# Kernel optimization log

Hardware: AMD Instinct MI355X
Metric: run time of the kernel (lower is better)

Reference implementation:

```python
import jax, jax.numpy as jnp
import numpy as np

EPS = 1e-8
BLOCK = 10  # proposals per frame; block-diagonal zeroing granularity


def _l2norm(x):
    # torch.norm(x, dim=-1, keepdim=True) + 1e-8
    return x / (jnp.linalg.norm(x, axis=-1, keepdims=True) + EPS)


def _block_mask(N):
    # For row j: zero cols [ (j//10)*10 , (j//10)*10 + 9 ) (i.e. 9 cols), then restore the diagonal.
    rows = jnp.arange(N)[:, None]
    cols = jnp.arange(N)[None, :]
    bstart = (rows // BLOCK) * BLOCK
    zeroed = (cols >= bstart) & (cols < bstart + (BLOCK - 1))
    keep = (~zeroed) | (rows == cols)
    return keep.astype(jnp.float32)  # [N, N]


def setup_inputs() -> dict:
    key = jax.random.key(0)
    k1, k2, k3, k4 = jax.random.split(key, 4)
    B, N, C = 1, 2000, 256
    x_cls = jax.random.normal(k1, (B, N, C), dtype=jnp.float32)
    x_reg = jax.random.normal(k2, (B, N, C), dtype=jnp.float32)
    s = 1.0 / np.sqrt(C)
    W_qkv_cls = jax.random.uniform(k3, (C, 3 * C), dtype=jnp.float32, minval=-s, maxval=s)
    W_qkv_reg = jax.random.uniform(k4, (C, 3 * C), dtype=jnp.float32, minval=-s, maxval=s)
    return {"x_cls": x_cls, "x_reg": x_reg, "W_qkv_cls": W_qkv_cls, "W_qkv_reg": W_qkv_reg}


def reference(x_cls, x_reg, W_qkv_cls, W_qkv_reg):
    num_heads = 8
    scale = 25.0
    sim_thresh = 0.75
    B, N, C = x_cls.shape
    hd = C // num_heads

    def qkv(x, W):
        # [B,N,3C] -> (3,B,H,N,hd)
        t = (x @ W).reshape(B, N, 3, num_heads, hd)
        return jnp.transpose(t, (2, 0, 3, 1, 4))

    q_cls, k_cls, v_cls = qkv(x_cls, W_qkv_cls)
    q_reg, k_reg, _v_reg = qkv(x_reg, W_qkv_reg)

    q_cls = _l2norm(q_cls)
    k_cls = _l2norm(k_cls)
    q_reg = _l2norm(q_reg)
    k_reg = _l2norm(k_reg)
    v_cls_normed = _l2norm(v_cls)

    # cosine-similarity of values (used for sim mask)
    attn_cls_raw = jnp.einsum('bhnd,bhmd->bhnm', v_cls_normed, v_cls_normed)

    attn_cls = jax.nn.softmax(jnp.einsum('bhnd,bhmd->bhnm', q_cls, k_cls) * scale, axis=-1)
    attn_reg = jax.nn.softmax(jnp.einsum('bhnd,bhmd->bhnm', q_reg, k_reg) * scale, axis=-1)
    attn = (attn_reg + attn_cls) * 0.5

    # block-diagonal zeroing (keeps diagonal), replacing the original CPU/numpy loop
    attn = attn * _block_mask(N)[None, None, :, :]

    x = jnp.einsum('bhnm,bhmd->bhnd', attn, v_cls)
    x = jnp.transpose(x, (0, 2, 1, 3)).reshape(B, N, C)
    x_ori = jnp.transpose(v_cls, (0, 2, 1, 3)).reshape(B, N, C)
    x_out = jnp.concatenate([x, x_ori], axis=-1)  # [B, N, 2C]

    # ave=True branch
    raw_mean = jnp.sum(attn_cls_raw, axis=1)[0] / num_heads          # [N, N]
    sim_mask = (raw_mean > sim_thresh).astype(jnp.float32)
    sim_attn = jnp.sum(attn, axis=1)[0] / num_heads                   # [N, N]
    sim_round2 = jax.nn.softmax(sim_attn, axis=-1)
    sim_round2 = sim_mask * sim_round2 / (jnp.sum(sim_mask * sim_round2, axis=-1, keepdims=True) + EPS)

    return (x_out, sim_round2)
```

## Files before the change

### kernel.cpp

```cpp
#include <hip/hip_runtime.h>
#include <math.h>

#define N_TOK 2000
#define NH 8
#define NHH 2
#define HD 32
#define SCALE 25.0f
#define SIM_TH 0.75f
#define EPSF 1e-8f
#define NT 125
#define QT 16

typedef _Float16 half2_t __attribute__((ext_vector_type(2)));
typedef _Float16 f16x4 __attribute__((ext_vector_type(4)));
typedef _Float16 f16x8 __attribute__((ext_vector_type(8)));
typedef float f32x4 __attribute__((ext_vector_type(4)));

__device__ __forceinline__ half2_t u2h(unsigned u) {
  return __builtin_bit_cast(half2_t, u);
}
__device__ __forceinline__ unsigned h2u(half2_t h) {
  return __builtin_bit_cast(unsigned, h);
}

__device__ __forceinline__ float block_max256(float v, float* red) {
#pragma unroll
  for (int off = 32; off > 0; off >>= 1) v = fmaxf(v, __shfl_xor(v, off, 64));
  __syncthreads();
  if ((threadIdx.x & 63) == 0) red[threadIdx.x >> 6] = v;
  __syncthreads();
  return fmaxf(fmaxf(red[0], red[1]), fmaxf(red[2], red[3]));
}
__device__ __forceinline__ float block_sum256(float v, float* red) {
#pragma unroll
  for (int off = 32; off > 0; off >>= 1) v += __shfl_xor(v, off, 64);
  __syncthreads();
  if ((threadIdx.x & 63) == 0) red[threadIdx.x >> 6] = v;
  __syncthreads();
  return (red[0] + red[1]) + (red[2] + red[3]);
}

__global__ __launch_bounds__(256) void wpackT_kernel(
    const float* __restrict__ W_cls, const float* __restrict__ W_reg,
    _Float16* __restrict__ Wt_cls, _Float16* __restrict__ Wt_reg) {
  const int idx = blockIdx.x * 256 + threadIdx.x;
  const int kc = idx / 768;
  const int n = idx % 768;
  const float* __restrict__ W = blockIdx.y ? W_reg : W_cls;
  _Float16* __restrict__ Wt = blockIdx.y ? Wt_reg : Wt_cls;
  uint4 o;
  o.x = h2u((half2_t){(_Float16)W[(kc * 8 + 0) * 768 + n],
                      (_Float16)W[(kc * 8 + 1) * 768 + n]});
  o.y = h2u((half2_t){(_Float16)W[(kc * 8 + 2) * 768 + n],
                      (_Float16)W[(kc * 8 + 3) * 768 + n]});
  o.z = h2u((half2_t){(_Float16)W[(kc * 8 + 4) * 768 + n],
                      (_Float16)W[(kc * 8 + 5) * 768 + n]});
  o.w = h2u((half2_t){(_Float16)W[(kc * 8 + 6) * 768 + n],
                      (_Float16)W[(kc * 8 + 7) * 768 + n]});
  *(uint4*)(Wt + (size_t)n * 256 + kc * 8) = o;
}

__global__ __launch_bounds__(256) void qkv_mfma_kernel(
    const float* __restrict__ x_cls, const float* __restrict__ x_reg,
    const _Float16* __restrict__ Wt_cls, const _Float16* __restrict__ Wt_reg,
    _Float16* __restrict__ qc2, _Float16* __restrict__ qr2,
    _Float16* __restrict__ kc2, _Float16* __restrict__ kr2,
    _Float16* __restrict__ vn2, float* __restrict__ v_rm,
    _Float16* __restrict__ v_t) {
  __shared__ _Float16 xs[16][264];

  const int tid = threadIdx.x;
  const int c = blockIdx.y;
  const int which = (c >= 3) ? 1 : 0;
  const int sec = which ? (c - 3) : c;
  const int n0 = sec * 256;
  const int i0 = blockIdx.x * 16;
  const float* __restrict__ x = which ? x_reg : x_cls;
  const _Float16* __restrict__ Wt = which ? Wt_reg : Wt_cls;

  {
    const int tok = tid >> 4, c4 = tid & 15;
    const float4* __restrict__ xr =
        (const float4*)(x + (size_t)(i0 + tok) * 256);
#pragma unroll
    for (int r = 0; r < 4; r++) {
      const float4 v = xr[c4 + 16 * r];
      *(unsigned*)&xs[tok][(c4 + 16 * r) * 4] =
          h2u((half2_t){(_Float16)v.x, (_Float16)v.y});
      *(unsigned*)&xs[tok][(c4 + 16 * r) * 4 + 2] =
          h2u((half2_t){(_Float16)v.z, (_Float16)v.w});
    }
  }
  __syncthreads();

  const int w = tid >> 6, l = tid & 63;
  const int q = l & 15, kg = l >> 4;
  const f32x4 zero4 = {0.f, 0.f, 0.f, 0.f};
  f32x4 acc[4] = {zero4, zero4, zero4, zero4};
  const int nb = n0 + w * 64;

#pragma unroll
  for (int ks = 0; ks < 8; ks++) {
    const int k0 = ks * 32;
    const f16x8 bx = *(const f16x8*)&xs[q][k0 + kg * 8];
#pragma unroll
    for (int t2 = 0; t2 < 4; t2++) {
      const f16x8 aw = *(const f16x8*)(
          Wt + (size_t)(nb + t2 * 16 + q) * 256 + k0 + kg * 8);
      acc[t2] =
          __builtin_amdgcn_mfma_f32_16x16x32_f16(aw, bx, acc[t2], 0, 0, 0);
    }
  }

  float ss0 = 0.f, ss1 = 0.f;
#pragma unroll
  for (int i = 0; i < 4; i++) {
    ss0 += acc[0][i] * acc[0][i] + acc[1][i] * acc[1][i];
    ss1 += acc[2][i] * acc[2][i] + acc[3][i] * acc[3][i];
  }
  ss0 += __shfl_xor(ss0, 16, 64);
  ss0 += __shfl_xor(ss0, 32, 64);
  ss1 += __shfl_xor(ss1, 16, 64);
  ss1 += __shfl_xor(ss1, 32, 64);
  const float inv0 = 1.0f / (sqrtf(ss0) + EPSF);
  const float inv1 = 1.0f / (sqrtf(ss1) + EPSF);

  const int tok = i0 + q;
#pragma unroll
  for (int t2 = 0; t2 < 4; t2++) {
    const float inv = (t2 < 2) ? inv0 : inv1;
    const int nrel = w * 64 + t2 * 16 + kg * 4;
    const int h = nrel >> 5, d0 = nrel & 31;
    uint2 un;
    un.x = h2u((half2_t){(_Float16)(acc[t2][0] * inv),
                         (_Float16)(acc[t2][1] * inv)});
    un.y = h2u((half2_t){(_Float16)(acc[t2][2] * inv),
                         (_Float16)(acc[t2][3] * inv)});
    const size_t off = ((size_t)(h * N_TOK) + tok) * 32 + d0;
    if (sec == 0) {
      *(uint2*)((which ? qr2 : qc2) + off) = un;
    } else if (sec == 1) {
      *(uint2*)((which ? kr2 : kc2) + off) = un;
    } else {
      *(uint2*)(vn2 + off) = un;
      const float4 vr = {acc[t2][0], acc[t2][1], acc[t2][2], acc[t2][3]};
      *(float4*)(v_rm + off) = vr;
#pragma unroll
      for (int i = 0; i < 4; i++) {
        v_t[((size_t)(h * 32) + d0 + i) * N_TOK + tok] = (_Float16)acc[t2][i];
      }
    }
  }
}

__global__ __launch_bounds__(256) void attn33_kernel(
    const _Float16* __restrict__ qc2, const _Float16* __restrict__ qr2,
    const _Float16* __restrict__ kc2, const _Float16* __restrict__ kr2,
    const _Float16* __restrict__ vn2, const _Float16* __restrict__ v_t,
    const float* __restrict__ v_rm, float* __restrict__ out_x,
    _Float16* __restrict__ sim_ws, _Float16* __restrict__ raw_ws) {
  __shared__ _Float16 qst[3][NHH][QT][40];
  __shared__ float smem_u[4224];

  float* __restrict__ sums_l = smem_u;
  float* __restrict__ nrm = smem_u + 256;
  float* __restrict__ st = smem_u;
  float* __restrict__ pvr = smem_u;

  const int tid = threadIdx.x;
  const int w = tid >> 6;
  const int l = tid & 63;
  const int qgrp = blockIdx.x >> 2;
  const int hp = blockIdx.x & 3;
  const int hq = hp * NHH;
  const int i0 = qgrp * QT;
  _Float16* __restrict__ simp = sim_ws + (size_t)hp * N_TOK * N_TOK;
  _Float16* __restrict__ rawp = raw_ws + (size_t)hp * N_TOK * N_TOK;

  if (tid < 128) {
    const int hh = tid >> 6, row = (tid >> 2) & 15, dg = tid & 3;
    const size_t src =
        ((size_t)((hq + hh) * N_TOK) + (i0 + row)) * HD + dg * 8;
    *(uint4*)&qst[0][hh][row][dg * 8] = *(const uint4*)(qc2 + src);
    *(uint4*)&qst[1][hh][row][dg * 8] = *(const uint4*)(qr2 + src);
    *(uint4*)&qst[2][hh][row][dg * 8] = *(const uint4*)(vn2 + src);
  }
  __syncthreads();

  const int q = l & 15;
  const int kg = l >> 4;
  const int i_glob = i0 + q;
  const int bs = (i_glob / 10) * 10;

  const f32x4 zero4 = {0.f, 0.f, 0.f, 0.f};

  float sc[NHH], sr[NHH];
#pragma unroll
  for (int hh = 0; hh < NHH; hh++) { sc[hh] = 0.f; sr[hh] = 0.f; }

  for (int t = w; t < NT; t += 4) {
    const int mb = t * 16;
#pragma unroll
    for (int hh = 0; hh < NHH; hh++) {
      const size_t koff =
          ((size_t)((hq + hh) * N_TOK) + mb + q) * HD + kg * 8;
      const f16x8 akc = *(const f16x8*)(kc2 + koff);
      const f16x8 akr = *(const f16x8*)(kr2 + koff);
      const f16x8 bqc = *(const f16x8*)&qst[0][hh][q][kg * 8];
      const f16x8 bqr = *(const f16x8*)&qst[1][hh][q][kg * 8];
      const f32x4 dc =
          __builtin_amdgcn_mfma_f32_16x16x32_f16(akc, bqc, zero4, 0, 0, 0);
      const f32x4 dr =
          __builtin_amdgcn_mfma_f32_16x16x32_f16(akr, bqr, zero4, 0, 0, 0);
#pragma unroll
      for (int i = 0; i < 4; i++) {
        sc[hh] += __expf(dc[i] * SCALE - SCALE);
        sr[hh] += __expf(dr[i] * SCALE - SCALE);
      }
    }
  }
#pragma unroll
  for (int hh = 0; hh < NHH; hh++) {
    sc[hh] += __shfl_xor(sc[hh], 16, 64);
    sc[hh] += __shfl_xor(sc[hh], 32, 64);
    sr[hh] += __shfl_xor(sr[hh], 16, 64);
    sr[hh] += __shfl_xor(sr[hh], 32, 64);
  }
  if (l < 16) {
#pragma unroll
    for (int hh = 0; hh < NHH; hh++) {
      sums_l[((w * 2 + 0) * NHH + hh) * 16 + l] = sc[hh];
      sums_l[((w * 2 + 1) * NHH + hh) * 16 + l] = sr[hh];
    }
  }
  __syncthreads();
  if (tid < 64) {
    const int pl = tid >> 5, hh = (tid >> 4) & 1, qq = tid & 15;
    const float s = sums_l[((0 * 2 + pl) * NHH + hh) * 16 + qq] +
                    sums_l[((1 * 2 + pl) * NHH + hh) * 16 + qq] +
                    sums_l[((2 * 2 + pl) * NHH + hh) * 16 + qq] +
                    sums_l[((3 * 2 + pl) * NHH + hh) * 16 + qq];
    nrm[(pl * NHH + hh) * 16 + qq] = 0.5f / s;
  }
  __syncthreads();
  float ncr[NHH], nrr[NHH];
#pragma unroll
  for (int hh = 0; hh < NHH; hh++) {
    ncr[hh] = nrm[(0 * NHH + hh) * 16 + q];
    nrr[hh] = nrm[(1 * NHH + hh) * 16 + q];
  }
  __syncthreads();

  f32x4 pv[NHH][2];
#pragma unroll
  for (int hh = 0; hh < NHH; hh++) { pv[hh][0] = zero4; pv[hh][1] = zero4; }

  for (int t = w; t < NT; t += 4) {
    const int mb = t * 16;
    f32x4 simt = zero4;
    f32x4 rawt = zero4;
#pragma unroll
    for (int hh = 0; hh < NHH; hh++) {
      const int h = hq + hh;
      const size_t koff = ((size_t)(h * N_TOK) + mb + q) * HD + kg * 8;
      const f16x8 akc = *(const f16x8*)(kc2 + koff);
      const f16x8 akr = *(const f16x8*)(kr2 + koff);
      const f16x8 avn = *(const f16x8*)(vn2 + koff);
      const f16x8 bqc = *(const f16x8*)&qst[0][hh][q][kg * 8];
      const f16x8 bqr = *(const f16x8*)&qst[1][hh][q][kg * 8];
      const f16x8 bqv = *(const f16x8*)&qst[2][hh][q][kg * 8];
      const f32x4 dc =
          __builtin_amdgcn_mfma_f32_16x16x32_f16(akc, bqc, zero4, 0, 0, 0);
      const f32x4 dr =
          __builtin_amdgcn_mfma_f32_16x16x32_f16(akr, bqr, zero4, 0, 0, 0);
      rawt = __builtin_amdgcn_mfma_f32_16x16x32_f16(avn, bqv, rawt, 0, 0, 0);

      f16x4 pa;
#pragma unroll
      for (int i = 0; i < 4; i++) {
        const float ec = __expf(dc[i] * SCALE - SCALE);
        const float er = __expf(dr[i] * SCALE - SCALE);
        float ai = ncr[hh] * ec + nrr[hh] * er;
        const int m = mb + kg * 4 + i;
        if (m >= bs && m < bs + 9 && m != i_glob) ai = 0.f;
        simt[i] += ai;
        pa[i] = (_Float16)ai;
      }
      const f16x4 bv0 = *(const f16x4*)(
          v_t + ((size_t)(h * HD) + q) * N_TOK + mb + kg * 4);
      const f16x4 bv1 = *(const f16x4*)(
          v_t + ((size_t)(h * HD) + 16 + q) * N_TOK + mb + kg * 4);
      pv[hh][0] =
          __builtin_amdgcn_mfma_f32_16x16x16f16(pa, bv0, pv[hh][0], 0, 0, 0);
      pv[hh][1] =
          __builtin_amdgcn_mfma_f32_16x16x16f16(pa, bv1, pv[hh][1], 0, 0, 0);
    }
    st[(w * 16 + q) * 20 + kg * 4 + 0] = simt[0];
    st[(w * 16 + q) * 20 + kg * 4 + 1] = simt[1];
    st[(w * 16 + q) * 20 + kg * 4 + 2] = simt[2];
    st[(w * 16 + q) * 20 + kg * 4 + 3] = simt[3];
    {
      const int row = l >> 2, mo = (l & 3) * 4;
      const float4 v4 = *(const float4*)&st[(w * 16 + row) * 20 + mo];
      uint2 u;
      u.x = h2u((half2_t){(_Float16)v4.x, (_Float16)v4.y});
      u.y = h2u((half2_t){(_Float16)v4.z, (_Float16)v4.w});
      *(uint2*)(simp + (size_t)(i0 + row) * N_TOK + mb + mo) = u;
    }
    st[(w * 16 + q) * 20 + kg * 4 + 0] = rawt[0];
    st[(w * 16 + q) * 20 + kg * 4 + 1] = rawt[1];
    st[(w * 16 + q) * 20 + kg * 4 + 2] = rawt[2];
    st[(w * 16 + q) * 20 + kg * 4 + 3] = rawt[3];
    {
      const int row = l >> 2, mo = (l & 3) * 4;
      const float4 v4 = *(const float4*)&st[(w * 16 + row) * 20 + mo];
      uint2 u;
      u.x = h2u((half2_t){(_Float16)v4.x, (_Float16)v4.y});
      u.y = h2u((half2_t){(_Float16)v4.z, (_Float16)v4.w});
      *(uint2*)(rawp + (size_t)(i0 + row) * N_TOK + mb + mo) = u;
    }
  }

  __syncthreads();
#pragma unroll
  for (int hh = 0; hh < NHH; hh++) {
#pragma unroll
    for (int i = 0; i < 4; i++) {
      pvr[((w * 2 + hh) * 16 + kg * 4 + i) * 33 + q] = pv[hh][0][i];
      pvr[((w * 2 + hh) * 16 + kg * 4 + i) * 33 + 16 + q] = pv[hh][1][i];
    }
  }
  __syncthreads();
  {
    const int hh = tid >> 7, qg2 = (tid >> 5) & 3, d = tid & 31;
#pragma unroll
    for (int qi = 0; qi < 4; qi++) {
      const int qq = qg2 * 4 + qi;
      float s = 0.f;
#pragma unroll
      for (int wv = 0; wv < 4; wv++) {
        s += pvr[((wv * 2 + hh) * 16 + qq) * 33 + d];
      }
      out_x[(size_t)(i0 + qq) * 512 + (hq + hh) * 32 + d] = s;
    }
  }
  if (tid < 64) {
    const int hh = tid >> 5, d = tid & 31;
    const int h = hq + hh;
#pragma unroll
    for (int qq = 0; qq < QT; qq++) {
      out_x[(size_t)(i0 + qq) * 512 + 256 + h * 32 + d] =
          v_rm[((size_t)(h * N_TOK) + i0 + qq) * HD + d];
    }
  }
}

__global__ __launch_bounds__(256) void sim_round2_kernel(
    const _Float16* __restrict__ sim_ws, const _Float16* __restrict__ raw_ws,
    float* __restrict__ out_sim) {
  __shared__ float red[16];
  const int tid = threadIdx.x;
  const size_t NN = (size_t)N_TOK * N_TOK;
  const bool act = tid < 250;
#pragma unroll
  for (int r = 0; r < 2; r++) {
    const int i = blockIdx.x * 2 + r;
    float s[8], rw[8];
    if (act) {
      const size_t base = (size_t)i * N_TOK + tid * 8;
      const f16x8 s0 = *(const f16x8*)(sim_ws + base);
      const f16x8 s1 = *(const f16x8*)(sim_ws + NN + base);
      const f16x8 s2 = *(const f16x8*)(sim_ws + 2 * NN + base);
      const f16x8 s3 = *(const f16x8*)(sim_ws + 3 * NN + base);
      const f16x8 r0 = *(const f16x8*)(raw_ws + base);
      const f16x8 r1 = *(const f16x8*)(raw_ws + NN + base);
      const f16x8 r2 = *(const f16x8*)(raw_ws + 2 * NN + base);
      const f16x8 r3 = *(const f16x8*)(raw_ws + 3 * NN + base);
#pragma unroll
      for (int e = 0; e < 8; e++) {
        s[e] = ((float)s0[e] + (float)s1[e] + (float)s2[e] + (float)s3[e]) *
               0.125f;
        rw[e] = (float)r0[e] + (float)r1[e] + (float)r2[e] + (float)r3[e];
      }
    } else {
#pragma unroll
      for (int e = 0; e < 8; e++) { s[e] = -1e30f; rw[e] = 0.f; }
    }
    float lm = -1e30f;
#pragma unroll
    for (int e = 0; e < 8; e++) lm = fmaxf(lm, s[e]);
    const float M = block_max256(lm, red);
    float ls = 0.f;
#pragma unroll
    for (int e = 0; e < 8; e++) {
      const float ev = __expf(s[e] - M);
      s[e] = ev;
      ls += ev;
    }
    const float S = block_sum256(ls, red);
    const float invS = 1.0f / S;
    float lms = 0.f;
#pragma unroll
    for (int e = 0; e < 8; e++) {
      const float p = s[e] * invS;
      const float mp = (act && (rw[e] * 0.125f > SIM_TH)) ? p : 0.f;
      s[e] = mp;
      lms += mp;
    }
    const float MS = block_sum256(lms, red);
    const float invMS = 1.0f / (MS + EPSF);
    if (act) {
      float* __restrict__ outp = out_sim + (size_t)i * N_TOK + tid * 8;
      const float4 o0 = {s[0] * invMS, s[1] * invMS, s[2] * invMS,
                         s[3] * invMS};
      const float4 o1 = {s[4] * invMS, s[5] * invMS, s[6] * invMS,
                         s[7] * invMS};
      *(float4*)outp = o0;
      *(float4*)(outp + 4) = o1;
    }
  }
}

extern "C" void kernel_launch(void* const* d_in, const int* in_sizes, int n_in,
                              void* d_out, int out_size, void* d_ws,
                              size_t ws_size, hipStream_t stream) {
  const float* x_cls = (const float*)d_in[0];
  const float* x_reg = (const float*)d_in[1];
  const float* W_cls = (const float*)d_in[2];
  const float* W_reg = (const float*)d_in[3];

  const size_t seg = (size_t)NH * N_TOK * HD;
  float* v_rm = (float*)d_ws;
  _Float16* qc2 = (_Float16*)(v_rm + seg);
  _Float16* qr2 = qc2 + seg;
  _Float16* kc2 = qr2 + seg;
  _Float16* kr2 = kc2 + seg;
  _Float16* vn2 = kr2 + seg;
  _Float16* v_t = vn2 + seg;
  _Float16* sim_ws = v_t + seg;
  _Float16* raw_ws = sim_ws + 4 * (size_t)N_TOK * N_TOK;
  _Float16* Wt_cls = raw_ws + 4 * (size_t)N_TOK * N_TOK;
  _Float16* Wt_reg = Wt_cls + 768 * 256;

  dim3 g0(96, 2);
  wpackT_kernel<<<g0, 256, 0, stream>>>(W_cls, W_reg, Wt_cls, Wt_reg);

  dim3 g1(125, 5);
  qkv_mfma_kernel<<<g1, 256, 0, stream>>>(x_cls, x_reg, Wt_cls, Wt_reg, qc2,
                                          qr2, kc2, kr2, vn2, v_rm, v_t);

  float* out_x = (float*)d_out;
  float* out_sim = out_x + (size_t)N_TOK * 512;
  attn33_kernel<<<500, 256, 0, stream>>>(qc2, qr2, kc2, kr2, vn2, v_t, v_rm,
                                         out_x, sim_ws, raw_ws);
  sim_round2_kernel<<<1000, 256, 0, stream>>>(sim_ws, raw_ws, out_sim);
}
```

Before: 162.6 us.

## Split attention over key halves into separate sum and PV kernels

Splits the fused attention kernel into two kernels that each split the key dimension in half across blocks, doubling the grid from 500 to 1000 blocks. The first kernel computes the softmax denominators per key half and writes them to a workspace. The second combines them and computes the sim/raw tiles plus partial PV results. The final kernel sums the two PV partials and copies v into the output. This aims to raise occupancy and parallelism on a large GPU, at the cost of an extra launch, recomputing QK in both passes, and extra workspace traffic.

```diff
diff --git a/kernel.cpp b/kernel.cpp
--- a/kernel.cpp
+++ b/kernel.cpp
@@ -9,6 +9,7 @@
 #define SIM_TH 0.75f
 #define EPSF 1e-8f
 #define NT 125
+#define NTS 63
 #define QT 16
 
 typedef _Float16 half2_t __attribute__((ext_vector_type(2)));
@@ -153,29 +154,21 @@
   }
 }
 
-__global__ __launch_bounds__(256) void attn33_kernel(
+__global__ __launch_bounds__(256) void attn_p1_kernel(
     const _Float16* __restrict__ qc2, const _Float16* __restrict__ qr2,
     const _Float16* __restrict__ kc2, const _Float16* __restrict__ kr2,
-    const _Float16* __restrict__ vn2, const _Float16* __restrict__ v_t,
-    const float* __restrict__ v_rm, float* __restrict__ out_x,
-    _Float16* __restrict__ sim_ws, _Float16* __restrict__ raw_ws) {
-  __shared__ _Float16 qst[3][NHH][QT][40];
-  __shared__ float smem_u[4224];
-
-  float* __restrict__ sums_l = smem_u;
-  float* __restrict__ nrm = smem_u + 256;
-  float* __restrict__ st = smem_u;
-  float* __restrict__ pvr = smem_u;
+    float* __restrict__ sums_ws) {
+  __shared__ _Float16 qst[2][NHH][QT][40];
+  __shared__ float sums_l[4][2][NHH][16];
 
   const int tid = threadIdx.x;
   const int w = tid >> 6;
   const int l = tid & 63;
-  const int qgrp = blockIdx.x >> 2;
-  const int hp = blockIdx.x & 3;
+  const int qgrp = blockIdx.x >> 3;
+  const int hp = (blockIdx.x >> 1) & 3;
+  const int kh = blockIdx.x & 1;
   const int hq = hp * NHH;
   const int i0 = qgrp * QT;
-  _Float16* __restrict__ simp = sim_ws + (size_t)hp * N_TOK * N_TOK;
-  _Float16* __restrict__ rawp = raw_ws + (size_t)hp * N_TOK * N_TOK;
 
   if (tid < 128) {
     const int hh = tid >> 6, row = (tid >> 2) & 15, dg = tid & 3;
@@ -183,22 +176,19 @@
         ((size_t)((hq + hh) * N_TOK) + (i0 + row)) * HD + dg * 8;
     *(uint4*)&qst[0][hh][row][dg * 8] = *(const uint4*)(qc2 + src);
     *(uint4*)&qst[1][hh][row][dg * 8] = *(const uint4*)(qr2 + src);
-    *(uint4*)&qst[2][hh][row][dg * 8] = *(const uint4*)(vn2 + src);
-  }
-  __syncthreads();
-
-  const int q = l & 15;
-  const int kg = l >> 4;
-  const int i_glob = i0 + q;
-  const int bs = (i_glob / 10) * 10;
-
+  }
+  __syncthreads();
+
+  const int q = l & 15, kg = l >> 4;
   const f32x4 zero4 = {0.f, 0.f, 0.f, 0.f};
 
   float sc[NHH], sr[NHH];
 #pragma unroll
   for (int hh = 0; hh < NHH; hh++) { sc[hh] = 0.f; sr[hh] = 0.f; }
 
-  for (int t = w; t < NT; t += 4) {
+  const int t0 = kh ? NTS : 0;
+  const int t1 = kh ? NT : NTS;
+  for (int t = t0 + w; t < t1; t += 4) {
     const int mb = t * 16;
 #pragma unroll
     for (int hh = 0; hh < NHH; hh++) {
@@ -229,20 +219,65 @@
   if (l < 16) {
 #pragma unroll
     for (int hh = 0; hh < NHH; hh++) {
-      sums_l[((w * 2 + 0) * NHH + hh) * 16 + l] = sc[hh];
-      sums_l[((w * 2 + 1) * NHH + hh) * 16 + l] = sr[hh];
+      sums_l[w][0][hh][l] = sc[hh];
+      sums_l[w][1][hh][l] = sr[hh];
     }
   }
   __syncthreads();
   if (tid < 64) {
     const int pl = tid >> 5, hh = (tid >> 4) & 1, qq = tid & 15;
-    const float s = sums_l[((0 * 2 + pl) * NHH + hh) * 16 + qq] +
-                    sums_l[((1 * 2 + pl) * NHH + hh) * 16 + qq] +
-                    sums_l[((2 * 2 + pl) * NHH + hh) * 16 + qq] +
-                    sums_l[((3 * 2 + pl) * NHH + hh) * 16 + qq];
+    const float s = sums_l[0][pl][hh][qq] + sums_l[1][pl][hh][qq] +
+                    sums_l[2][pl][hh][qq] + sums_l[3][pl][hh][qq];
+    sums_ws[((size_t)(kh * 2 + pl) * NH + hq + hh) * N_TOK + i0 + qq] = s;
+  }
+}
+
+__global__ __launch_bounds__(256) void attn_p2_kernel(
+    const _Float16* __restrict__ qc2, const _Float16* __restrict__ qr2,
+    const _Float16* __restrict__ kc2, const _Float16* __restrict__ kr2,
+    const _Float16* __restrict__ vn2, const _Float16* __restrict__ v_t,
+    const float* __restrict__ sums_ws, float* __restrict__ pv_ws,
+    _Float16* __restrict__ sim_ws, _Float16* __restrict__ raw_ws) {
+  __shared__ _Float16 qst[3][NHH][QT][40];
+  __shared__ float smem_u[4224];
+
+  float* __restrict__ nrm = smem_u + 3584;
+  float* __restrict__ st = smem_u;
+  float* __restrict__ pvr = smem_u;
+
+  const int tid = threadIdx.x;
+  const int w = tid >> 6;
+  const int l = tid & 63;
+  const int qgrp = blockIdx.x >> 3;
+  const int hp = (blockIdx.x >> 1) & 3;
+  const int kh = blockIdx.x & 1;
+  const int hq = hp * NHH;
+  const int i0 = qgrp * QT;
+  _Float16* __restrict__ simp = sim_ws + (size_t)hp * N_TOK * N_TOK;
+  _Float16* __restrict__ rawp = raw_ws + (size_t)hp * N_TOK * N_TOK;
+
+  if (tid < 128) {
+    const int hh = tid >> 6, row = (tid >> 2) & 15, dg = tid & 3;
+    const size_t src =
+        ((size_t)((hq + hh) * N_TOK) + (i0 + row)) * HD + dg * 8;
+    *(uint4*)&qst[0][hh][row][dg * 8] = *(const uint4*)(qc2 + src);
+    *(uint4*)&qst[1][hh][row][dg * 8] = *(const uint4*)(qr2 + src);
+    *(uint4*)&qst[2][hh][row][dg * 8] = *(const uint4*)(vn2 + src);
+  }
+  if (tid < 64) {
+    const int pl = tid >> 5, hh = (tid >> 4) & 1, qq = tid & 15;
+    const size_t base = ((size_t)pl * NH + hq + hh) * N_TOK + i0 + qq;
+    const float s =
+        sums_ws[base] + sums_ws[(size_t)2 * NH * N_TOK + base];
     nrm[(pl * NHH + hh) * 16 + qq] = 0.5f / s;
   }
   __syncthreads();
+
+  const int q = l & 15;
+  const int kg = l >> 4;
+  const int i_glob = i0 + q;
+  const int bs = (i_glob / 10) * 10;
+
   float ncr[NHH], nrr[NHH];
 #pragma unroll
   for (int hh = 0; hh < NHH; hh++) {
@@ -251,11 +286,14 @@
   }
   __syncthreads();
 
+  const f32x4 zero4 = {0.f, 0.f, 0.f, 0.f};
   f32x4 pv[NHH][2];
 #pragma unroll
   for (int hh = 0; hh < NHH; hh++) { pv[hh][0] = zero4; pv[hh][1] = zero4; }
 
-  for (int t = w; t < NT; t += 4) {
+  const int t0 = kh ? NTS : 0;
+  const int t1 = kh ? NT : NTS;
+  for (int t = t0 + w; t < t1; t += 4) {
     const int mb = t * 16;
     f32x4 simt = zero4;
     f32x4 rawt = zero4;
@@ -341,30 +379,29 @@
       for (int wv = 0; wv < 4; wv++) {
         s += pvr[((wv * 2 + hh) * 16 + qq) * 33 + d];
       }
-      out_x[(size_t)(i0 + qq) * 512 + (hq + hh) * 32 + d] = s;
-    }
-  }
-  if (tid < 64) {
-    const int hh = tid >> 5, d = tid & 31;
-    const int h = hq + hh;
-#pragma unroll
-    for (int qq = 0; qq < QT; qq++) {
-      out_x[(size_t)(i0 + qq) * 512 + 256 + h * 32 + d] =
-          v_rm[((size_t)(h * N_TOK) + i0 + qq) * HD + d];
+      pv_ws[(size_t)kh * N_TOK * 256 + (size_t)(i0 + qq) * 256 +
+            (hq + hh) * 32 + d] = s;
     }
   }
 }
 
 __global__ __launch_bounds__(256) void sim_round2_kernel(
     const _Float16* __restrict__ sim_ws, const _Float16* __restrict__ raw_ws,
-    float* __restrict__ out_sim) {
+    const float* __restrict__ pv_ws, const float* __restrict__ v_rm,
+    float* __restrict__ out_x, float* __restrict__ out_sim) {
   __shared__ float red[16];
   const int tid = threadIdx.x;
   const size_t NN = (size_t)N_TOK * N_TOK;
+  const size_t PVN = (size_t)N_TOK * 256;
   const bool act = tid < 250;
 #pragma unroll
   for (int r = 0; r < 2; r++) {
     const int i = blockIdx.x * 2 + r;
+    out_x[(size_t)i * 512 + tid] =
+        pv_ws[(size_t)i * 256 + tid] + pv_ws[PVN + (size_t)i * 256 + tid];
+    out_x[(size_t)i * 512 + 256 + tid] =
+        v_rm[((size_t)(tid >> 5) * N_TOK + i) * 32 + (tid & 31)];
+
     float s[8], rw[8];
     if (act) {
       const size_t base = (size_t)i * N_TOK + tid * 8;
@@ -441,6 +478,8 @@
   _Float16* raw_ws = sim_ws + 4 * (size_t)N_TOK * N_TOK;
   _Float16* Wt_cls = raw_ws + 4 * (size_t)N_TOK * N_TOK;
   _Float16* Wt_reg = Wt_cls + 768 * 256;
+  float* sums_ws = (float*)(Wt_reg + 768 * 256);
+  float* pv_ws = sums_ws + 4 * NH * N_TOK;
 
   dim3 g0(96, 2);
   wpackT_kernel<<<g0, 256, 0, stream>>>(W_cls, W_reg, Wt_cls, Wt_reg);
@@ -451,7 +490,9 @@
 
   float* out_x = (float*)d_out;
   float* out_sim = out_x + (size_t)N_TOK * 512;
-  attn33_kernel<<<500, 256, 0, stream>>>(qc2, qr2, kc2, kr2, vn2, v_t, v_rm,
-                                         out_x, sim_ws, raw_ws);
-  sim_round2_kernel<<<1000, 256, 0, stream>>>(sim_ws, raw_ws, out_sim);
-}
+  attn_p1_kernel<<<1000, 256, 0, stream>>>(qc2, qr2, kc2, kr2, sums_ws);
+  attn_p2_kernel<<<1000, 256, 0, stream>>>(qc2, qr2, kc2, kr2, vn2, v_t,
+                                           sums_ws, pv_ws, sim_ws, raw_ws);
+  sim_round2_kernel<<<1000, 256, 0, stream>>>(sim_ws, raw_ws, pv_ws, v_rm,
+                                              out_x, out_sim);
+}
```

Result: faster. 155.9 us (-4.1%).

## Split attention into softmax-sum and apply kernels with 512-thread blocks

Applied to the files above, without the earlier changes.

The fused attention kernel is split into two launches. The first computes the softmax denominators and writes them to a workspace buffer. The second reads them and does the masked attention, PV product and similarity outputs. Both kernels now use 8 waves per block instead of 4, so each wave handles half as many key tiles. This adds a launch and a small global round trip for the sums, and uses more shared memory per block.

```diff
diff --git a/kernel.cpp b/kernel.cpp
--- a/kernel.cpp
+++ b/kernel.cpp
@@ -153,19 +153,12 @@
   }
 }
 
-__global__ __launch_bounds__(256) void attn33_kernel(
+__global__ __launch_bounds__(512) void attn_p1_kernel(
     const _Float16* __restrict__ qc2, const _Float16* __restrict__ qr2,
     const _Float16* __restrict__ kc2, const _Float16* __restrict__ kr2,
-    const _Float16* __restrict__ vn2, const _Float16* __restrict__ v_t,
-    const float* __restrict__ v_rm, float* __restrict__ out_x,
-    _Float16* __restrict__ sim_ws, _Float16* __restrict__ raw_ws) {
-  __shared__ _Float16 qst[3][NHH][QT][40];
-  __shared__ float smem_u[4224];
-
-  float* __restrict__ sums_l = smem_u;
-  float* __restrict__ nrm = smem_u + 256;
-  float* __restrict__ st = smem_u;
-  float* __restrict__ pvr = smem_u;
+    float* __restrict__ sums_ws) {
+  __shared__ _Float16 qst[2][NHH][QT][40];
+  __shared__ float sums_l[8][2][NHH][16];
 
   const int tid = threadIdx.x;
   const int w = tid >> 6;
@@ -174,8 +167,6 @@
   const int hp = blockIdx.x & 3;
   const int hq = hp * NHH;
   const int i0 = qgrp * QT;
-  _Float16* __restrict__ simp = sim_ws + (size_t)hp * N_TOK * N_TOK;
-  _Float16* __restrict__ rawp = raw_ws + (size_t)hp * N_TOK * N_TOK;
 
   if (tid < 128) {
     const int hh = tid >> 6, row = (tid >> 2) & 15, dg = tid & 3;
@@ -183,22 +174,17 @@
         ((size_t)((hq + hh) * N_TOK) + (i0 + row)) * HD + dg * 8;
     *(uint4*)&qst[0][hh][row][dg * 8] = *(const uint4*)(qc2 + src);
     *(uint4*)&qst[1][hh][row][dg * 8] = *(const uint4*)(qr2 + src);
-    *(uint4*)&qst[2][hh][row][dg * 8] = *(const uint4*)(vn2 + src);
-  }
-  __syncthreads();
-
-  const int q = l & 15;
-  const int kg = l >> 4;
-  const int i_glob = i0 + q;
-  const int bs = (i_glob / 10) * 10;
-
+  }
+  __syncthreads();
+
+  const int q = l & 15, kg = l >> 4;
   const f32x4 zero4 = {0.f, 0.f, 0.f, 0.f};
 
   float sc[NHH], sr[NHH];
 #pragma unroll
   for (int hh = 0; hh < NHH; hh++) { sc[hh] = 0.f; sr[hh] = 0.f; }
 
-  for (int t = w; t < NT; t += 4) {
+  for (int t = w; t < NT; t += 8) {
     const int mb = t * 16;
 #pragma unroll
     for (int hh = 0; hh < NHH; hh++) {
@@ -229,20 +215,64 @@
   if (l < 16) {
 #pragma unroll
     for (int hh = 0; hh < NHH; hh++) {
-      sums_l[((w * 2 + 0) * NHH + hh) * 16 + l] = sc[hh];
-      sums_l[((w * 2 + 1) * NHH + hh) * 16 + l] = sr[hh];
+      sums_l[w][0][hh][l] = sc[hh];
+      sums_l[w][1][hh][l] = sr[hh];
     }
   }
   __syncthreads();
   if (tid < 64) {
     const int pl = tid >> 5, hh = (tid >> 4) & 1, qq = tid & 15;
-    const float s = sums_l[((0 * 2 + pl) * NHH + hh) * 16 + qq] +
-                    sums_l[((1 * 2 + pl) * NHH + hh) * 16 + qq] +
-                    sums_l[((2 * 2 + pl) * NHH + hh) * 16 + qq] +
-                    sums_l[((3 * 2 + pl) * NHH + hh) * 16 + qq];
+    float s = 0.f;
+#pragma unroll
+    for (int wv = 0; wv < 8; wv++) s += sums_l[wv][pl][hh][qq];
+    sums_ws[((size_t)pl * NH + hq + hh) * N_TOK + i0 + qq] = s;
+  }
+}
+
+__global__ __launch_bounds__(512) void attn_p2_kernel(
+    const _Float16* __restrict__ qc2, const _Float16* __restrict__ qr2,
+    const _Float16* __restrict__ kc2, const _Float16* __restrict__ kr2,
+    const _Float16* __restrict__ vn2, const _Float16* __restrict__ v_t,
+    const float* __restrict__ sums_ws, const float* __restrict__ v_rm,
+    float* __restrict__ out_x,
+    _Float16* __restrict__ sim_ws, _Float16* __restrict__ raw_ws) {
+  __shared__ _Float16 qst[3][NHH][QT][40];
+  __shared__ float smem_u[8448];
+
+  float* __restrict__ nrm = smem_u + 8384;
+  float* __restrict__ st = smem_u;
+  float* __restrict__ pvr = smem_u;
+
+  const int tid = threadIdx.x;
+  const int w = tid >> 6;
+  const int l = tid & 63;
+  const int qgrp = blockIdx.x >> 2;
+  const int hp = blockIdx.x & 3;
+  const int hq = hp * NHH;
+  const int i0 = qgrp * QT;
+  _Float16* __restrict__ simp = sim_ws + (size_t)hp * N_TOK * N_TOK;
+  _Float16* __restrict__ rawp = raw_ws + (size_t)hp * N_TOK * N_TOK;
+
+  if (tid < 128) {
+    const int hh = tid >> 6, row = (tid >> 2) & 15, dg = tid & 3;
+    const size_t src =
+        ((size_t)((hq + hh) * N_TOK) + (i0 + row)) * HD + dg * 8;
+    *(uint4*)&qst[0][hh][row][dg * 8] = *(const uint4*)(qc2 + src);
+    *(uint4*)&qst[1][hh][row][dg * 8] = *(const uint4*)(qr2 + src);
+    *(uint4*)&qst[2][hh][row][dg * 8] = *(const uint4*)(vn2 + src);
+  }
+  if (tid < 64) {
+    const int pl = tid >> 5, hh = (tid >> 4) & 1, qq = tid & 15;
+    const float s = sums_ws[((size_t)pl * NH + hq + hh) * N_TOK + i0 + qq];
     nrm[(pl * NHH + hh) * 16 + qq] = 0.5f / s;
   }
   __syncthreads();
+
+  const int q = l & 15;
+  const int kg = l >> 4;
+  const int i_glob = i0 + q;
+  const int bs = (i_glob / 10) * 10;
+
   float ncr[NHH], nrr[NHH];
 #pragma unroll
   for (int hh = 0; hh < NHH; hh++) {
@@ -251,11 +281,12 @@
   }
   __syncthreads();
 
+  const f32x4 zero4 = {0.f, 0.f, 0.f, 0.f};
   f32x4 pv[NHH][2];
 #pragma unroll
   for (int hh = 0; hh < NHH; hh++) { pv[hh][0] = zero4; pv[hh][1] = zero4; }
 
-  for (int t = w; t < NT; t += 4) {
+  for (int t = w; t < NT; t += 8) {
     const int mb = t * 16;
     f32x4 simt = zero4;
     f32x4 rawt = zero4;
@@ -332,13 +363,14 @@
   }
   __syncthreads();
   {
-    const int hh = tid >> 7, qg2 = (tid >> 5) & 3, d = tid & 31;
-#pragma unroll
-    for (int qi = 0; qi < 4; qi++) {
-      const int qq = qg2 * 4 + qi;
+    const int hh = tid >> 8, rem = tid & 255;
+    const int qq2 = rem >> 5, d = rem & 31;
+#pragma unroll
+    for (int qi = 0; qi < 2; qi++) {
+      const int qq = qq2 * 2 + qi;
       float s = 0.f;
 #pragma unroll
-      for (int wv = 0; wv < 4; wv++) {
+      for (int wv = 0; wv < 8; wv++) {
         s += pvr[((wv * 2 + hh) * 16 + qq) * 33 + d];
       }
       out_x[(size_t)(i0 + qq) * 512 + (hq + hh) * 32 + d] = s;
@@ -441,6 +473,7 @@
   _Float16* raw_ws = sim_ws + 4 * (size_t)N_TOK * N_TOK;
   _Float16* Wt_cls = raw_ws + 4 * (size_t)N_TOK * N_TOK;
   _Float16* Wt_reg = Wt_cls + 768 * 256;
+  float* sums_ws = (float*)(Wt_reg + 768 * 256);
 
   dim3 g0(96, 2);
   wpackT_kernel<<<g0, 256, 0, stream>>>(W_cls, W_reg, Wt_cls, Wt_reg);
@@ -451,7 +484,9 @@
 
   float* out_x = (float*)d_out;
   float* out_sim = out_x + (size_t)N_TOK * 512;
-  attn33_kernel<<<500, 256, 0, stream>>>(qc2, qr2, kc2, kr2, vn2, v_t, v_rm,
-                                         out_x, sim_ws, raw_ws);
+  attn_p1_kernel<<<500, 512, 0, stream>>>(qc2, qr2, kc2, kr2, sums_ws);
+  attn_p2_kernel<<<500, 512, 0, stream>>>(qc2, qr2, kc2, kr2, vn2, v_t,
+                                          sums_ws, v_rm, out_x, sim_ws,
+                                          raw_ws);
   sim_round2_kernel<<<1000, 256, 0, stream>>>(sim_ws, raw_ws, out_sim);
 }
```

After: 158.9 us. -2.2%, faster.
